# Optimization experiments

Measured on AMD Instinct MI355X. Metric: run time of the kernel, lower is better.

The kernel has to match this reference:

```python
import jax, jax.numpy as jnp
import numpy as np

S, B, T, H, K, FH, OUT = 4, 256, 256, 128, 5, 48, 1
DW, AW = 64, 32            # dynamics-MLP width, attention width
EPS_BN, EPS_U = 1e-5, 1e-6


def setup_inputs() -> dict:
    key = jax.random.key(0)
    ks = jax.random.split(key, 16)
    r = lambda i, shape, s: jax.random.normal(ks[i], shape, jnp.float32) * s
    return {
        "x": jax.random.normal(ks[0], (B, 1, T), jnp.float32),
        "t_span": jnp.linspace(0.0, 1.0, T, dtype=jnp.float32),
        # decomposer: per-scale DynamicDilationConv + BN + ReLU + Conv1d + BN + ReLU
        "c1w": r(1, (S, 1, 1, K), 0.3), "c1b": jnp.zeros((S, 1)),
        "bn1_g": jnp.ones((S, 1)), "bn1_b": jnp.zeros((S, 1)),
        "c2w": r(2, (S, 1, 1, K), 0.3), "c2b": jnp.zeros((S, 1)),
        "bn2_g": jnp.ones((S, 1)), "bn2_b": jnp.zeros((S, 1)),
        # per-scale ProbabilisticNeuralDynamics MLP: (H+1+1) -> 64 -> 2H
        "dw1": r(3, (S, H + 2, DW), 0.1), "db1": jnp.zeros((S, DW)),
        "dw2": r(4, (S, DW, 2 * H), 0.1), "db2": jnp.zeros((S, 2 * H)),
        # fusion attention H -> 32 -> 1
        "a1w": r(5, (H, AW), 0.1), "a1b": jnp.zeros((AW,)),
        "a2w": r(6, (AW, 1), 0.1), "a2b": jnp.zeros((1,)),
        # GRU (torch layout: W_ih [3H, in], W_hh [3H, H])
        "wih": r(7, (3 * H, OUT), 0.1), "whh": r(8, (3 * H, H), 0.05),
        "bih": jnp.zeros((3 * H,)), "bhh": jnp.zeros((3 * H,)),
        "fcw": r(9, (H, OUT), 0.1), "fcb": jnp.zeros((OUT,)),
        "lvw": r(10, (H, OUT), 0.1), "lvb": jnp.zeros((OUT,)),
        "init_token": jnp.zeros((1, OUT)),
    }


def _conv1d(x, w, b):
    # x:[B,C,L], w:[O,I,K]; dilation = round(clamp(exp(log_dilation=0),1)) = 1
    pad = (w.shape[-1] - 1) // 2
    y = jax.lax.conv_general_dilated(x, w, (1,), [(pad, pad)],
                                     dimension_numbers=("NCH", "OIH", "NCH"))
    return y + b[None, :, None]


def _bn(x, g, b):
    # BatchNorm1d in training mode: batch stats over (N, L)
    m = x.mean(axis=(0, 2), keepdims=True)
    v = x.var(axis=(0, 2), keepdims=True)
    return g[None, :, None] * (x - m) * jax.lax.rsqrt(v + EPS_BN) + b[None, :, None]


def _decompose(x, c1w, c1b, g1, b1, c2w, c2b, g2, b2):
    h = jnp.maximum(_bn(_conv1d(x, c1w, c1b), g1, b1), 0.0)
    h = jnp.maximum(_bn(_conv1d(h, c2w, c2b), g2, b2), 0.0)
    return h  # [B,1,T]


def _ode_scale(xseq, t_span, w1, b1, w2, b2):
    # xseq:[B,T,1]; integrate (mu, logvar) with RK4 on the t_span grid
    def f(t, h):
        idx = jnp.argmin(jnp.abs(t_span - t))
        x_t = jnp.take(xseq, idx, axis=1)                 # [B,1]
        tf = t * jnp.ones((h.shape[0], 1), h.dtype)       # time feature
        u = jnp.maximum(jnp.concatenate([h, x_t, tf], -1) @ w1 + b1, 0.0) @ w2 + b2
        return u[:, :H], u[:, H:]

    def step(carry, ts):
        h, lv = carry
        t0, t1 = ts
        dt = t1 - t0
        k1m, k1v = f(t0, h)
        k2m, k2v = f(t0 + dt / 2, h + dt / 2 * k1m)
        k3m, k3v = f(t0 + dt / 2, h + dt / 2 * k2m)
        k4m, k4v = f(t1, h + dt * k3m)
        h = h + dt / 6 * (k1m + 2 * k2m + 2 * k3m + k4m)
        lv = lv + dt / 6 * (k1v + 2 * k2v + 2 * k3v + k4v)
        return (h, lv), None

    z = jnp.zeros((xseq.shape[0], H), xseq.dtype)
    (h, lv), _ = jax.lax.scan(step, (z, z), (t_span[:-1], t_span[1:]))
    return h, lv  # final-time latent, matching h_sol[:, -1, :]


def _forward(x, t_span, c1w, c1b, bn1_g, bn1_b, c2w, c2b, bn2_g, bn2_b,
             dw1, db1, dw2, db2, a1w, a1b, a2w, a2b,
             wih, whh, bih, bhh, fcw, fcb, lvw, lvb, init_token):
    # multi-scale decomposition -> [S,B,1,T]
    comps = jax.vmap(_decompose, in_axes=(None, 0, 0, 0, 0, 0, 0, 0, 0))(
        x, c1w, c1b, bn1_g, bn1_b, c2w, c2b, bn2_g, bn2_b)
    xseqs = comps[:, :, 0, :, None]                       # [S,B,T,1]
    means, logvars = jax.vmap(_ode_scale, in_axes=(0, None, 0, 0, 0, 0))(
        xseqs, t_span, dw1, db1, dw2, db2)                # each [S,B,H]
    means = jnp.transpose(means, (1, 0, 2))               # [B,S,H]
    logvars = jnp.transpose(logvars, (1, 0, 2))
    # uncertainty-scaled attention fusion
    scores = jnp.maximum(means @ a1w + a1b, 0.0) @ a2w + a2b        # [B,S,1]
    uncert = jnp.mean(jnp.exp(logvars), axis=-1, keepdims=True)     # [B,S,1]
    weights = jax.nn.softmax(scores / (uncert + EPS_U), axis=1)
    fused = jnp.sum(weights * means, axis=1)              # [B,H]

    def dec_step(carry, _):
        h, tok = carry
        gi = tok @ wih.T + bih
        gh = h @ whh.T + bhh
        ir, iz, inn = jnp.split(gi, 3, axis=-1)
        hr, hz, hn = jnp.split(gh, 3, axis=-1)
        r = jax.nn.sigmoid(ir + hr)
        zz = jax.nn.sigmoid(iz + hz)
        n = jnp.tanh(inn + r * hn)
        h = (1.0 - zz) * n + zz * h
        pred = h @ fcw + fcb
        plv = h @ lvw + lvb
        return (h, pred), (pred, plv)

    tok0 = jnp.broadcast_to(init_token, (fused.shape[0], OUT))
    _, (outs, lvs) = jax.lax.scan(dec_step, (fused, tok0), None, length=FH)
    return jnp.transpose(outs, (1, 0, 2)), jnp.transpose(lvs, (1, 0, 2))


def reference(x, t_span, c1w, c1b, bn1_g, bn1_b, c2w, c2b, bn2_g, bn2_b,
              dw1, db1, dw2, db2, a1w, a1b, a2w, a2b,
              wih, whh, bih, bhh, fcw, fcb, lvw, lvb, init_token):
    return _forward(x, t_span, c1w, c1b, bn1_g, bn1_b, c2w, c2b, bn2_g, bn2_b,
                    dw1, db1, dw2, db2, a1w, a1b, a2w, a2b,
                    wih, whh, bih, bhh, fcw, fcb, lvw, lvb, init_token)
```

## Files before the change

kernel.cpp:

```cpp
#include <hip/hip_runtime.h>
#include <math.h>

#define NS   4
#define NB   256
#define NT   256
#define NH   128
#define NDW  64
#define NFH  48

__global__ __launch_bounds__(256) void k_d1(
    const float* __restrict__ x,
    const float* __restrict__ c1w, const float* __restrict__ c1b,
    float* __restrict__ tmpA, double* __restrict__ pp1)
{
    const int s     = blockIdx.x >> 6;
    const int chunk = blockIdx.x & 63;
    const int tid   = threadIdx.x;
    __shared__ double wred[4][2];

    float w[5];
#pragma unroll
    for (int k = 0; k < 5; ++k) w[k] = c1w[s*5 + k];
    const float cb = c1b[s];

    double ls = 0.0, lq = 0.0;
#pragma unroll
    for (int r = 0; r < 4; ++r) {
        const int bb = chunk*4 + r;
        const float* xb = x + bb*NT;
        float acc = cb;
#pragma unroll
        for (int k = 0; k < 5; ++k) {
            int tt = tid + k - 2;
            if (tt >= 0 && tt < NT) acc += xb[tt] * w[k];
        }
        tmpA[s*65536 + bb*NT + tid] = acc;
        ls += (double)acc; lq += (double)acc * (double)acc;
    }
#pragma unroll
    for (int off = 32; off > 0; off >>= 1) {
        ls += __shfl_xor(ls, off); lq += __shfl_xor(lq, off);
    }
    if ((tid & 63) == 0) { wred[tid>>6][0] = ls; wred[tid>>6][1] = lq; }
    __syncthreads();
    if (tid == 0) {
        pp1[(s*64 + chunk)*2 + 0] = wred[0][0]+wred[1][0]+wred[2][0]+wred[3][0];
        pp1[(s*64 + chunk)*2 + 1] = wred[0][1]+wred[1][1]+wred[2][1]+wred[3][1];
    }
}

__global__ __launch_bounds__(256) void k_d3(
    const float* __restrict__ tmpA, const double* __restrict__ pp1,
    const float* __restrict__ g1,  const float* __restrict__ b1,
    const float* __restrict__ c2w, const float* __restrict__ c2b,
    float* __restrict__ cv2, double* __restrict__ pp2)
{
    const int s     = blockIdx.x >> 6;
    const int chunk = blockIdx.x & 63;
    const int tid   = threadIdx.x;
    __shared__ float hsh[256];
    __shared__ double wred[4][2];

    double lsum = 0.0, lsq = 0.0;
    for (int q = 0; q < 64; ++q) {
        lsum += pp1[(s*64 + q)*2 + 0];
        lsq  += pp1[(s*64 + q)*2 + 1];
    }
    const double Nn = 65536.0;
    double mm = lsum / Nn;
    double vv = lsq / Nn - mm*mm;
    const float m1 = (float)mm, rs1 = (float)(1.0 / sqrt(vv + 1e-5));
    const float A1 = g1[s]*rs1, B1 = b1[s] - g1[s]*m1*rs1;

    float w[5];
#pragma unroll
    for (int k = 0; k < 5; ++k) w[k] = c2w[s*5 + k];
    const float cb = c2b[s];

    double ls = 0.0, lq = 0.0;
    for (int r = 0; r < 4; ++r) {
        const int bb = chunk*4 + r;
        float y = tmpA[s*65536 + bb*NT + tid];
        hsh[tid] = fmaxf(fmaf(A1, y, B1), 0.f);
        __syncthreads();
        float acc = cb;
#pragma unroll
        for (int k = 0; k < 5; ++k) {
            int tt = tid + k - 2;
            if (tt >= 0 && tt < NT) acc += hsh[tt] * w[k];
        }
        cv2[s*65536 + bb*NT + tid] = acc;
        ls += (double)acc; lq += (double)acc * (double)acc;
        __syncthreads();
    }
#pragma unroll
    for (int off = 32; off > 0; off >>= 1) {
        ls += __shfl_xor(ls, off); lq += __shfl_xor(lq, off);
    }
    if ((tid & 63) == 0) { wred[tid>>6][0] = ls; wred[tid>>6][1] = lq; }
    __syncthreads();
    if (tid == 0) {
        pp2[(s*64 + chunk)*2 + 0] = wred[0][0]+wred[1][0]+wred[2][0]+wred[3][0];
        pp2[(s*64 + chunk)*2 + 1] = wred[0][1]+wred[1][1]+wred[2][1]+wred[3][1];
    }
}

__global__ __launch_bounds__(64) void k_mat(
    const float* __restrict__ dw1, const float* __restrict__ dw2,
    const float* __restrict__ db2, const float* __restrict__ tspan,
    float* __restrict__ Mt, float* __restrict__ bM,
    int* __restrict__ imid_g, float* __restrict__ Tg)
{
    if (blockIdx.x == 256) {
        __shared__ float ts[256];
        const int t = threadIdx.x;
        for (int e = t; e < 256; e += 64) ts[e] = tspan[e];
        __syncthreads();
        for (int i = t; i < 255; i += 64) {
            float t0 = ts[i], t1 = ts[i+1];
            float tm = t0 + (t1 - t0) * 0.5f;
            int best = 0; float bd = fabsf(ts[0] - tm);
            for (int j = 1; j < 256; ++j) {
                float d = fabsf(ts[j] - tm);
                if (d < bd) { bd = d; best = j; }
            }
            imid_g[i] = best;
        }
        if (t == 0) {
            float T = 0.f;
            for (int i = 0; i < 255; ++i) T += (ts[i+1] - ts[i]);
            Tg[0] = T;
        }
        return;
    }
    const int s = blockIdx.x >> 6;
    const int c = blockIdx.x & 63;
    const int k = threadIdx.x;
    __shared__ float col[128];

    col[k]      = dw1[(s*130 + k)*64 + c];
    col[k + 64] = dw1[(s*130 + 64 + k)*64 + c];
    __syncthreads();

    const float4* dp = (const float4*)(dw2 + (s*64 + k)*256);
    double acc = 0.0;
#pragma unroll 8
    for (int j4 = 0; j4 < 32; ++j4) {
        float4 dv = dp[j4];
        acc += (double)dv.x * (double)col[4*j4+0]
             + (double)dv.y * (double)col[4*j4+1]
             + (double)dv.z * (double)col[4*j4+2]
             + (double)dv.w * (double)col[4*j4+3];
    }
    const int slot = (k & 48) | (((c & 15) - (k & 15)) & 15);
    Mt[(s*64 + c)*64 + slot] = (float)acc;

    double pb = (double)db2[s*256 + k]      * (double)col[k]
              + (double)db2[s*256 + 64 + k] * (double)col[k + 64];
#pragma unroll
    for (int off = 32; off > 0; off >>= 1) pb += __shfl_xor(pb, off);
    if (k == 0) bM[s*64 + c] = (float)pb;
}

__device__ __forceinline__ float bperm(int addr, float v) {
    return __int_as_float(__builtin_amdgcn_ds_bpermute(addr, __float_as_int(v)));
}

#define FSTEP(p) \
    asm("v_fmac_f32 %0, %1, %2 row_ror:" #p " row_mask:0xf bank_mask:0xf" \
        : "+v"(d0) : "v"(u0), "v"(Mc[p])); \
    asm("v_fmac_f32 %0, %1, %2 row_ror:" #p " row_mask:0xf bank_mask:0xf" \
        : "+v"(d1) : "v"(u1), "v"(Mc[16+(p)])); \
    asm("v_fmac_f32 %0, %1, %2 row_ror:" #p " row_mask:0xf bank_mask:0xf" \
        : "+v"(d2) : "v"(u2), "v"(Mc[32+(p)])); \
    asm("v_fmac_f32 %0, %1, %2 row_ror:" #p " row_mask:0xf bank_mask:0xf" \
        : "+v"(d3) : "v"(u3), "v"(Mc[48+(p)]));

__device__ __forceinline__ float dotFDPP(float u, const float* __restrict__ Mc,
                                         float bMc, int A0, int A1, int A2, int A3)
{
    float u0 = bperm(A0, u), u1 = bperm(A1, u);
    float u2 = bperm(A2, u), u3 = bperm(A3, u);
    float d0 = fmaf(u0, Mc[0], bMc);
    float d1 = u1 * Mc[16];
    float d2 = u2 * Mc[32];
    float d3 = u3 * Mc[48];
    FSTEP(1)  FSTEP(2)  FSTEP(3)  FSTEP(4)  FSTEP(5)  FSTEP(6)  FSTEP(7)
    FSTEP(8)  FSTEP(9)  FSTEP(10) FSTEP(11) FSTEP(12) FSTEP(13) FSTEP(14)
    FSTEP(15)
    return (d0 + d1) + (d2 + d3);
}

__global__ __attribute__((amdgpu_waves_per_eu(1, 1)))
__launch_bounds__(64) void k_ode(
    const float* __restrict__ cv2, const double* __restrict__ pp2,
    const float* __restrict__ g2,  const float* __restrict__ b2,
    const float* __restrict__ tspan, const int* __restrict__ imid_g,
    const float* __restrict__ Mt, const float* __restrict__ bM_g,
    const float* __restrict__ dw1, const float* __restrict__ db1,
    float* __restrict__ S_g)
{
    const int b   = blockIdx.x;
    const int s   = b >> 8;
    const int row = b & 255;
    const int l   = threadIdx.x;

    __shared__ __align__(16) float xls[256];
    __shared__ __align__(16) float xms[256];

    double lsum = 0.0, lsq = 0.0;
    for (int q = 0; q < 64; ++q) {
        lsum += pp2[(s*64 + q)*2 + 0];
        lsq  += pp2[(s*64 + q)*2 + 1];
    }
    const double Nn = 65536.0;
    double mm = lsum / Nn;
    double vv = lsq / Nn - mm*mm;
    const float m2 = (float)mm, rs2 = (float)(1.0 / sqrt(vv + 1e-5));
    const float bnA = g2[s]*rs2, bnB = b2[s] - g2[s]*m2*rs2;

    const float* __restrict__ xrow = cv2 + (s*NB + row)*NT;
#pragma unroll
    for (int q = 0; q < 4; ++q)
        xls[64*q + l] = fmaxf(fmaf(bnA, xrow[64*q + l], bnB), 0.f);
    __syncthreads();
#pragma unroll
    for (int q = 0; q < 4; ++q) {
        int idx = 64*q + l;
        if (idx < 255) xms[idx] = xls[imid_g[idx]];
    }
    __syncthreads();

    const float bMc = bM_g[s*64 + l];
    const float b1c = db1[s*64 + l];
    const float w1x = dw1[(s*130 + 128)*64 + l];
    const float w1t = dw1[(s*130 + 129)*64 + l];

    float Mc[64];
    const float4* mp = (const float4*)(Mt + (s*64 + l)*64);
#pragma unroll
    for (int j = 0; j < 16; ++j) {
        float4 t = mp[j];
        Mc[4*j+0] = t.x; Mc[4*j+1] = t.y; Mc[4*j+2] = t.z; Mc[4*j+3] = t.w;
    }
#pragma unroll
    for (int j = 0; j < 64; ++j) asm volatile("" : "+v"(Mc[j]));

    const int lm = (l & 15) << 2;
    const int A0 = lm, A1 = lm + 64, A2 = lm + 128, A3 = lm + 192;

    float a = 0.f;
    float S = 0.f;

    for (int i = 0; i < 255; ++i) {
        const float t0 = tspan[i];
        const float t1 = tspan[i+1];
        const float dt = t1 - t0;
        const float tm = t0 + dt * 0.5f;
        const float hdt = dt * 0.5f;
        const float xi  = xls[i];
        const float x1v = xls[i+1];
        const float xm  = xms[i];

        float u11 = fmaxf(a + b1c + xi*w1x + t0*w1t, 0.f);
        float v1  = dotFDPP(u11, Mc, bMc, A0, A1, A2, A3);
        float u12 = fmaxf(fmaf(hdt, v1, a) + b1c + xm*w1x + tm*w1t, 0.f);
        float v2  = dotFDPP(u12, Mc, bMc, A0, A1, A2, A3);
        float u13 = fmaxf(fmaf(hdt, v2, a) + b1c + xm*w1x + tm*w1t, 0.f);
        float v3  = dotFDPP(u13, Mc, bMc, A0, A1, A2, A3);
        float u14 = fmaxf(fmaf(dt, v3, a) + b1c + x1v*w1x + t1*w1t, 0.f);
        float v4  = dotFDPP(u14, Mc, bMc, A0, A1, A2, A3);

        float d6 = dt * (1.0f / 6.0f);
        a += d6 * ((v1 + v4) + 2.f*(v2 + v3));
        S += d6 * ((u11 + u14) + 2.f*(u12 + u13));
    }

    S_g[(s*256 + row)*64 + l] = S;
}

__global__ __launch_bounds__(384, 1) void k_gru(
    const float* __restrict__ S_g, const float* __restrict__ dw2,
    const float* __restrict__ db2, const float* __restrict__ Tg,
    const float* __restrict__ a1w, const float* __restrict__ a1b,
    const float* __restrict__ a2w, const float* __restrict__ a2b,
    const float* __restrict__ wih, const float* __restrict__ whh,
    const float* __restrict__ bih, const float* __restrict__ bhh,
    const float* __restrict__ fcw, const float* __restrict__ fcb,
    const float* __restrict__ lvw, const float* __restrict__ lvb,
    const float* __restrict__ init_token, float* __restrict__ out)
{
    const int b   = blockIdx.x;
    const int tid = threadIdx.x;

    __shared__ __align__(16) float Ssh[4][64];
    __shared__ __align__(16) float msh[4][128];
    __shared__ __align__(16) float evs[4][128];
    __shared__ __align__(16) float hl[128];
    __shared__ float ghl[384];
    __shared__ float scoreL[4];
    __shared__ float unc_part[2][4];
    __shared__ float wgt[4];
    __shared__ float redL[2][2];
    __shared__ float tokL;

    if (tid < 256) {
        int s = tid >> 6, cc = tid & 63;
        Ssh[s][cc] = S_g[(s*256 + b)*64 + cc];
    }
    const float T = Tg[0];
    __syncthreads();

    for (int e = tid; e < 1024; e += 384) {
        int s = e >> 8, j = e & 255;
        float acc = T * db2[s*256 + j];
        const float4* s4 = (const float4*)Ssh[s];
#pragma unroll
        for (int k4 = 0; k4 < 16; ++k4) {
            float4 sv = s4[k4];
            acc += sv.x * dw2[(s*64 + 4*k4 + 0)*256 + j]
                 + sv.y * dw2[(s*64 + 4*k4 + 1)*256 + j]
                 + sv.z * dw2[(s*64 + 4*k4 + 2)*256 + j]
                 + sv.w * dw2[(s*64 + 4*k4 + 3)*256 + j];
        }
        if (j < 128) msh[s][j] = acc;
        else         evs[s][j - 128] = expf(acc);
    }
    __syncthreads();

    if (tid < 128) {
        int wv = tid >> 6;
#pragma unroll
        for (int s = 0; s < 4; ++s) {
            float v = evs[s][tid];
#pragma unroll
            for (int off = 32; off > 0; off >>= 1) v += __shfl_xor(v, off);
            if ((tid & 63) == 0) unc_part[wv][s] = v;
        }
    }
    if (tid < 128) {
        int s = tid >> 5, aq = tid & 31;
        float hd = a1b[aq];
#pragma unroll 4
        for (int i = 0; i < 128; ++i) hd += msh[s][i] * a1w[i*32 + aq];
        hd = fmaxf(hd, 0.f);
        float sc = hd * a2w[aq];
#pragma unroll
        for (int off = 16; off > 0; off >>= 1) sc += __shfl_xor(sc, off);
        if (aq == 0) scoreL[s] = sc + a2b[0];
    }
    __syncthreads();
    if (tid == 0) {
        float sv[4], mx = -1e30f;
#pragma unroll
        for (int s = 0; s < 4; ++s) {
            float u = (unc_part[0][s] + unc_part[1][s]) / 128.f;
            sv[s] = scoreL[s] / (u + 1e-6f);
            mx = fmaxf(mx, sv[s]);
        }
        float se = 0.f, ev[4];
#pragma unroll
        for (int s = 0; s < 4; ++s) { ev[s] = expf(sv[s] - mx); se += ev[s]; }
#pragma unroll
        for (int s = 0; s < 4; ++s) wgt[s] = ev[s] / se;
        tokL = init_token[0];
    }
    __syncthreads();
    if (tid < 128) {
        float f = 0.f;
#pragma unroll
        for (int s = 0; s < 4; ++s) f += wgt[s] * msh[s][tid];
        hl[tid] = f;
    }

    float4 whh4[32];
    const float4* wr = (const float4*)(whh + tid*128);
#pragma unroll
    for (int k = 0; k < 32; ++k) whh4[k] = wr[k];
    float bhhj = bhh[tid];
    float wih_r = 0.f, wih_z = 0.f, wih_n = 0.f;
    float bih_r = 0.f, bih_z = 0.f, bih_n = 0.f;
    float fcwi = 0.f, lvwi = 0.f;
    if (tid < 128) {
        wih_r = wih[tid]; wih_z = wih[128+tid]; wih_n = wih[256+tid];
        bih_r = bih[tid]; bih_z = bih[128+tid]; bih_n = bih[256+tid];
        fcwi  = fcw[tid]; lvwi  = lvw[tid];
    }
    const float fcbv = fcb[0], lvbv = lvb[0];
    __syncthreads();

    for (int t = 0; t < NFH; ++t) {
        float g0 = 0.f, g1 = 0.f, g2 = 0.f, g3 = 0.f;
        const float4* h4 = (const float4*)hl;
#pragma unroll
        for (int k = 0; k < 32; ++k) {
            float4 hv = h4[k];
            float4 wvv = whh4[k];
            g0 += hv.x * wvv.x; g1 += hv.y * wvv.y;
            g2 += hv.z * wvv.z; g3 += hv.w * wvv.w;
        }
        ghl[tid] = ((g0 + g1) + (g2 + g3)) + bhhj;
        __syncthreads();

        if (tid < 128) {
            float tok = tokL;
            float r  = 1.f / (1.f + expf(-(tok*wih_r + bih_r + ghl[tid])));
            float zz = 1.f / (1.f + expf(-(tok*wih_z + bih_z + ghl[128+tid])));
            float n  = tanhf(tok*wih_n + bih_n + r * ghl[256+tid]);
            float hn = (1.f - zz) * n + zz * hl[tid];
            hl[tid] = hn;
            float pp = hn * fcwi, pl = hn * lvwi;
#pragma unroll
            for (int off = 32; off > 0; off >>= 1) {
                pp += __shfl_xor(pp, off);
                pl += __shfl_xor(pl, off);
            }
            int wvx = tid >> 6;
            if ((tid & 63) == 0) { redL[wvx][0] = pp; redL[wvx][1] = pl; }
        }
        __syncthreads();
        if (tid == 0) {
            float pr = redL[0][0] + redL[1][0] + fcbv;
            float pv = redL[0][1] + redL[1][1] + lvbv;
            out[b*NFH + t] = pr;
            out[NB*NFH + b*NFH + t] = pv;
            tokL = pr;
        }
        __syncthreads();
    }
}

extern "C" void kernel_launch(void* const* d_in, const int* in_sizes, int n_in,
                              void* d_out, int out_size, void* d_ws, size_t ws_size,
                              hipStream_t stream)
{
    const float* x      = (const float*)d_in[0];
    const float* tspan  = (const float*)d_in[1];
    const float* c1w    = (const float*)d_in[2];
    const float* c1b    = (const float*)d_in[3];
    const float* bn1g   = (const float*)d_in[4];
    const float* bn1b   = (const float*)d_in[5];
    const float* c2w    = (const float*)d_in[6];
    const float* c2b    = (const float*)d_in[7];
    const float* bn2g   = (const float*)d_in[8];
    const float* bn2b   = (const float*)d_in[9];
    const float* dw1    = (const float*)d_in[10];
    const float* db1    = (const float*)d_in[11];
    const float* dw2    = (const float*)d_in[12];
    const float* db2    = (const float*)d_in[13];
    const float* a1w    = (const float*)d_in[14];
    const float* a1b    = (const float*)d_in[15];
    const float* a2w    = (const float*)d_in[16];
    const float* a2b    = (const float*)d_in[17];
    const float* wih    = (const float*)d_in[18];
    const float* whh    = (const float*)d_in[19];
    const float* bih    = (const float*)d_in[20];
    const float* bhh    = (const float*)d_in[21];
    const float* fcw    = (const float*)d_in[22];
    const float* fcb    = (const float*)d_in[23];
    const float* lvw    = (const float*)d_in[24];
    const float* lvb    = (const float*)d_in[25];
    const float* itok   = (const float*)d_in[26];

    float* ws    = (float*)d_ws;
    float*  cv2  = ws;
    float*  tmpA = ws + 262144;
    float*  S_g  = ws + 524288;
    float*  Mt   = ws + 589824;
    float*  bMg  = ws + 606208;
    float*  Tg   = ws + 606464;
    int*    imid = (int*)(ws + 606720);
    double* pp1  = (double*)(ws + 606976);
    double* pp2  = (double*)(ws + 608000);

    k_d1<<<256, 256, 0, stream>>>(x, c1w, c1b, tmpA, pp1);
    k_mat<<<257, 64, 0, stream>>>(dw1, dw2, db2, tspan, Mt, bMg, imid, Tg);
    k_d3<<<256, 256, 0, stream>>>(tmpA, pp1, bn1g, bn1b, c2w, c2b, cv2, pp2);
    k_ode<<<1024, 64, 0, stream>>>(cv2, pp2, bn2g, bn2b, tspan, imid,
                                   Mt, bMg, dw1, db1, S_g);
    k_gru<<<256, 384, 0, stream>>>(S_g, dw2, db2, Tg, a1w, a1b, a2w, a2b,
                                   wih, whh, bih, bhh, fcw, fcb, lvw, lvb,
                                   itok, (float*)d_out);
}
```

Measured before the change: 342.9 us.

## Split ODE matvec across two waves with LDS partial-sum exchange

The RK4 ODE kernel now runs 128 threads per block. Each wave holds half of the 64x64 dynamics matrix (32 registers instead of 64) and computes a partial dot product, and the two halves are combined through double-buffered shared memory with a barrier after each of the four matvecs per step. Time values are preloaded into registers and fetched with readlane, and x/t values for the next step are prefetched, replacing per-step global loads. This halves the serial DPP chain per wave and roughly doubles parallel lanes, but adds four block barriers and LDS round trips per step on the critical path.

```diff
diff --git a/kernel.cpp b/kernel.cpp
--- a/kernel.cpp
+++ b/kernel.cpp
@@ -162,38 +162,41 @@
     if (k == 0) bM[s*64 + c] = (float)pb;
 }
 
+__device__ __forceinline__ float rlf(float v, int l) {
+    return __int_as_float(__builtin_amdgcn_readlane(__float_as_int(v), l));
+}
+__device__ __forceinline__ float pick4f(float r0, float r1, float r2, float r3, int i) {
+    int l = i & 63, h = i >> 6;
+    float a = (h & 2) ? ((h & 1) ? r3 : r2) : ((h & 1) ? r1 : r0);
+    return rlf(a, l);
+}
 __device__ __forceinline__ float bperm(int addr, float v) {
     return __int_as_float(__builtin_amdgcn_ds_bpermute(addr, __float_as_int(v)));
 }
 
-#define FSTEP(p) \
+#define FSTEP2(p) \
     asm("v_fmac_f32 %0, %1, %2 row_ror:" #p " row_mask:0xf bank_mask:0xf" \
-        : "+v"(d0) : "v"(u0), "v"(Mc[p])); \
+        : "+v"(d0) : "v"(u0), "v"(McL[p])); \
     asm("v_fmac_f32 %0, %1, %2 row_ror:" #p " row_mask:0xf bank_mask:0xf" \
-        : "+v"(d1) : "v"(u1), "v"(Mc[16+(p)])); \
-    asm("v_fmac_f32 %0, %1, %2 row_ror:" #p " row_mask:0xf bank_mask:0xf" \
-        : "+v"(d2) : "v"(u2), "v"(Mc[32+(p)])); \
-    asm("v_fmac_f32 %0, %1, %2 row_ror:" #p " row_mask:0xf bank_mask:0xf" \
-        : "+v"(d3) : "v"(u3), "v"(Mc[48+(p)]));
-
-__device__ __forceinline__ float dotFDPP(float u, const float* __restrict__ Mc,
-                                         float bMc, int A0, int A1, int A2, int A3)
-{
-    float u0 = bperm(A0, u), u1 = bperm(A1, u);
-    float u2 = bperm(A2, u), u3 = bperm(A3, u);
-    float d0 = fmaf(u0, Mc[0], bMc);
-    float d1 = u1 * Mc[16];
-    float d2 = u2 * Mc[32];
-    float d3 = u3 * Mc[48];
-    FSTEP(1)  FSTEP(2)  FSTEP(3)  FSTEP(4)  FSTEP(5)  FSTEP(6)  FSTEP(7)
-    FSTEP(8)  FSTEP(9)  FSTEP(10) FSTEP(11) FSTEP(12) FSTEP(13) FSTEP(14)
-    FSTEP(15)
-    return (d0 + d1) + (d2 + d3);
-}
-
-__global__ __attribute__((amdgpu_waves_per_eu(1, 1)))
-__launch_bounds__(64) void k_ode(
-    const float* __restrict__ cv2, const double* __restrict__ pp2,
+        : "+v"(d1) : "v"(u1v), "v"(McL[16+(p)]));
+
+#define DOT(uin, vout) { \
+    float u0 = bperm(A0, (uin)), u1v = bperm(A1, (uin)); \
+    float d0 = fmaf(u0, McL[0], seed); \
+    float d1 = u1v * McL[16]; \
+    FSTEP2(1)  FSTEP2(2)  FSTEP2(3)  FSTEP2(4)  FSTEP2(5)  FSTEP2(6) \
+    FSTEP2(7)  FSTEP2(8)  FSTEP2(9)  FSTEP2(10) FSTEP2(11) FSTEP2(12) \
+    FSTEP2(13) FSTEP2(14) FSTEP2(15) \
+    float part = d0 + d1; \
+    pp[pb][w][l] = part; \
+    __syncthreads(); \
+    float oth = pp[pb][1 - w][l]; \
+    vout = part + oth; \
+    pb ^= 1; }
+
+__global__ __attribute__((amdgpu_waves_per_eu(2)))
+__launch_bounds__(128) void k_ode(
+    const float* __restrict__ cv2, const double* __restrict__ pp2g,
     const float* __restrict__ g2,  const float* __restrict__ b2,
     const float* __restrict__ tspan, const int* __restrict__ imid_g,
     const float* __restrict__ Mt, const float* __restrict__ bM_g,
@@ -203,80 +206,93 @@
     const int b   = blockIdx.x;
     const int s   = b >> 8;
     const int row = b & 255;
-    const int l   = threadIdx.x;
+    const int tid = threadIdx.x;
+    const int w   = tid >> 6;
+    const int l   = tid & 63;
 
     __shared__ __align__(16) float xls[256];
     __shared__ __align__(16) float xms[256];
+    __shared__ __align__(16) float pp[2][2][64];
 
     double lsum = 0.0, lsq = 0.0;
     for (int q = 0; q < 64; ++q) {
-        lsum += pp2[(s*64 + q)*2 + 0];
-        lsq  += pp2[(s*64 + q)*2 + 1];
+        lsum += pp2g[(s*64 + q)*2 + 0];
+        lsq  += pp2g[(s*64 + q)*2 + 1];
     }
     const double Nn = 65536.0;
-    double mm = lsum / Nn;
-    double vv = lsq / Nn - mm*mm;
-    const float m2 = (float)mm, rs2 = (float)(1.0 / sqrt(vv + 1e-5));
+    double mmv = lsum / Nn;
+    double vvv = lsq / Nn - mmv*mmv;
+    const float m2 = (float)mmv, rs2 = (float)(1.0 / sqrt(vvv + 1e-5));
     const float bnA = g2[s]*rs2, bnB = b2[s] - g2[s]*m2*rs2;
 
     const float* __restrict__ xrow = cv2 + (s*NB + row)*NT;
-#pragma unroll
-    for (int q = 0; q < 4; ++q)
-        xls[64*q + l] = fmaxf(fmaf(bnA, xrow[64*q + l], bnB), 0.f);
-    __syncthreads();
-#pragma unroll
-    for (int q = 0; q < 4; ++q) {
-        int idx = 64*q + l;
-        if (idx < 255) xms[idx] = xls[imid_g[idx]];
-    }
-    __syncthreads();
+    for (int e = tid; e < 256; e += 128)
+        xls[e] = fmaxf(fmaf(bnA, xrow[e], bnB), 0.f);
+    __syncthreads();
+    for (int e = tid; e < 255; e += 128)
+        xms[e] = xls[imid_g[e]];
 
     const float bMc = bM_g[s*64 + l];
     const float b1c = db1[s*64 + l];
     const float w1x = dw1[(s*130 + 128)*64 + l];
     const float w1t = dw1[(s*130 + 129)*64 + l];
-
-    float Mc[64];
-    const float4* mp = (const float4*)(Mt + (s*64 + l)*64);
-#pragma unroll
-    for (int j = 0; j < 16; ++j) {
+    const float seed = (w == 0) ? bMc : 0.0f;
+
+    float tr0 = tspan[l],       tr1 = tspan[64 + l];
+    float tr2 = tspan[128 + l], tr3 = tspan[192 + l];
+
+    float McL[32];
+    const float4* mp = (const float4*)(Mt + (s*64 + l)*64 + 32*w);
+#pragma unroll
+    for (int j = 0; j < 8; ++j) {
         float4 t = mp[j];
-        Mc[4*j+0] = t.x; Mc[4*j+1] = t.y; Mc[4*j+2] = t.z; Mc[4*j+3] = t.w;
-    }
-#pragma unroll
-    for (int j = 0; j < 64; ++j) asm volatile("" : "+v"(Mc[j]));
+        McL[4*j+0] = t.x; McL[4*j+1] = t.y; McL[4*j+2] = t.z; McL[4*j+3] = t.w;
+    }
+#pragma unroll
+    for (int j = 0; j < 32; ++j) asm volatile("" : "+v"(McL[j]));
 
     const int lm = (l & 15) << 2;
-    const int A0 = lm, A1 = lm + 64, A2 = lm + 128, A3 = lm + 192;
-
-    float a = 0.f;
-    float S = 0.f;
+    const int A0 = lm + 128*w;
+    const int A1 = lm + 64 + 128*w;
+
+    __syncthreads();
+
+    float a = 0.f, S = 0.f;
+    float t0  = rlf(tr0, 0);
+    float t1  = rlf(tr0, 1);
+    float xi  = xls[0], xmv = xms[0], x1v = xls[1];
+    int   pb  = 0;
 
     for (int i = 0; i < 255; ++i) {
-        const float t0 = tspan[i];
-        const float t1 = tspan[i+1];
-        const float dt = t1 - t0;
-        const float tm = t0 + dt * 0.5f;
+        float xin = 0.f, xmn = 0.f, x1n = 0.f, t1n = 0.f;
+        if (i < 254) {
+            xin = xls[i+1]; xmn = xms[i+1]; x1n = xls[i+2];
+            t1n = pick4f(tr0, tr1, tr2, tr3, i + 2);
+        }
+        const float dt  = t1 - t0;
+        const float tm  = t0 + dt * 0.5f;
         const float hdt = dt * 0.5f;
-        const float xi  = xls[i];
-        const float x1v = xls[i+1];
-        const float xm  = xms[i];
-
-        float u11 = fmaxf(a + b1c + xi*w1x + t0*w1t, 0.f);
-        float v1  = dotFDPP(u11, Mc, bMc, A0, A1, A2, A3);
-        float u12 = fmaxf(fmaf(hdt, v1, a) + b1c + xm*w1x + tm*w1t, 0.f);
-        float v2  = dotFDPP(u12, Mc, bMc, A0, A1, A2, A3);
-        float u13 = fmaxf(fmaf(hdt, v2, a) + b1c + xm*w1x + tm*w1t, 0.f);
-        float v3  = dotFDPP(u13, Mc, bMc, A0, A1, A2, A3);
-        float u14 = fmaxf(fmaf(dt, v3, a) + b1c + x1v*w1x + t1*w1t, 0.f);
-        float v4  = dotFDPP(u14, Mc, bMc, A0, A1, A2, A3);
+        const float c0  = b1c + xi*w1x  + t0*w1t;
+        const float cm  = b1c + xmv*w1x + tm*w1t;
+        const float c1  = b1c + x1v*w1x + t1*w1t;
+
+        float u11 = fmaxf(a + c0, 0.f);
+        float v1;  DOT(u11, v1)
+        float u12 = fmaxf(fmaf(hdt, v1, a) + cm, 0.f);
+        float v2;  DOT(u12, v2)
+        float u13 = fmaxf(fmaf(hdt, v2, a) + cm, 0.f);
+        float v3;  DOT(u13, v3)
+        float u14 = fmaxf(fmaf(dt, v3, a) + c1, 0.f);
+        float v4;  DOT(u14, v4)
 
         float d6 = dt * (1.0f / 6.0f);
         a += d6 * ((v1 + v4) + 2.f*(v2 + v3));
         S += d6 * ((u11 + u14) + 2.f*(u12 + u13));
-    }
-
-    S_g[(s*256 + row)*64 + l] = S;
+
+        t0 = t1; t1 = t1n; xi = xin; xmv = xmn; x1v = x1n;
+    }
+
+    if (w == 0) S_g[(s*256 + row)*64 + l] = S;
 }
 
 __global__ __launch_bounds__(384, 1) void k_gru(
@@ -409,14 +425,14 @@
             float n  = tanhf(tok*wih_n + bih_n + r * ghl[256+tid]);
             float hn = (1.f - zz) * n + zz * hl[tid];
             hl[tid] = hn;
-            float pp = hn * fcwi, pl = hn * lvwi;
+            float pg = hn * fcwi, pl = hn * lvwi;
 #pragma unroll
             for (int off = 32; off > 0; off >>= 1) {
-                pp += __shfl_xor(pp, off);
+                pg += __shfl_xor(pg, off);
                 pl += __shfl_xor(pl, off);
             }
             int wvx = tid >> 6;
-            if ((tid & 63) == 0) { redL[wvx][0] = pp; redL[wvx][1] = pl; }
+            if ((tid & 63) == 0) { redL[wvx][0] = pg; redL[wvx][1] = pl; }
         }
         __syncthreads();
         if (tid == 0) {
@@ -476,8 +492,8 @@
     k_d1<<<256, 256, 0, stream>>>(x, c1w, c1b, tmpA, pp1);
     k_mat<<<257, 64, 0, stream>>>(dw1, dw2, db2, tspan, Mt, bMg, imid, Tg);
     k_d3<<<256, 256, 0, stream>>>(tmpA, pp1, bn1g, bn1b, c2w, c2b, cv2, pp2);
-    k_ode<<<1024, 64, 0, stream>>>(cv2, pp2, bn2g, bn2b, tspan, imid,
-                                   Mt, bMg, dw1, db1, S_g);
+    k_ode<<<1024, 128, 0, stream>>>(cv2, pp2, bn2g, bn2b, tspan, imid,
+                                    Mt, bMg, dw1, db1, S_g);
     k_gru<<<256, 384, 0, stream>>>(S_g, dw2, db2, Tg, a1w, a1b, a2w, a2b,
                                    wih, whh, bih, bhh, fcw, fcb, lvw, lvb,
                                    itok, (float*)d_out);
```

Result: slower. 406.3 us (+18.5%).
